# Performance work log

Hardware: AMD Instinct MI355X
Metric: run time of the kernel (lower is better)

## Reference

```python
import jax, jax.numpy as jnp
from jax import lax
import numpy as np

B, C, H, W = 2, 64, 192, 192

def conv2d(x, w, pad):
    return lax.conv_general_dilated(x, w, (1, 1), [(pad, pad), (pad, pad)],
                                    dimension_numbers=('NCHW', 'OIHW', 'NCHW'))

def bilinear_sample(x, py, px):
    # x: [B,C,H,W]; py, px: [B,H,W] absolute fractional coords; zero padding outside.
    Bb, Cc, Hh, Ww = x.shape
    y0 = jnp.floor(py); x0 = jnp.floor(px)
    wy1 = py - y0; wx1 = px - x0
    xf = x.reshape(Bb, Cc, Hh * Ww)
    def gather(yi, xi):
        valid = (yi >= 0) & (yi < Hh) & (xi >= 0) & (xi < Ww)
        yc = jnp.clip(yi, 0, Hh - 1).astype(jnp.int32)
        xc = jnp.clip(xi, 0, Ww - 1).astype(jnp.int32)
        idx = (yc * Ww + xc).reshape(Bb, 1, Hh * Ww)
        v = jnp.take_along_axis(xf, idx, axis=2).reshape(Bb, Cc, Hh, Ww)
        return v * valid[:, None].astype(x.dtype)
    return (gather(y0, x0) * ((1 - wy1) * (1 - wx1))[:, None]
            + gather(y0, x0 + 1) * ((1 - wy1) * wx1)[:, None]
            + gather(y0 + 1, x0) * (wy1 * (1 - wx1))[:, None]
            + gather(y0 + 1, x0 + 1) * (wy1 * wx1)[:, None])

def deform_conv(x, w_off, b_off, w_mod, b_mod, w_reg, k):
    # torchvision deform_conv2d semantics with modulation (mask), stride=1, dilation=1.
    pad = k // 2
    offset = conv2d(x, w_off, pad) + b_off[None, :, None, None]   # [B,2*k*k,H,W] (y,x) interleaved
    mask = 2.0 * jax.nn.sigmoid(conv2d(x, w_mod, pad) + b_mod[None, :, None, None])  # [B,k*k,H,W]
    Bb, Cc, Hh, Ww = x.shape
    gy = jnp.arange(Hh, dtype=x.dtype)[None, :, None]
    gx = jnp.arange(Ww, dtype=x.dtype)[None, None, :]
    out = jnp.zeros((Bb, w_reg.shape[0], Hh, Ww), x.dtype)
    for i in range(k):          # fixed structural loop over kernel taps
        for j in range(k):
            t = i * k + j
            py = gy - pad + i + offset[:, 2 * t]
            px = gx - pad + j + offset[:, 2 * t + 1]
            samp = bilinear_sample(x, py, px) * mask[:, t][:, None]  # [B,C,H,W]
            out = out + jnp.einsum('bchw,oc->bohw', samp, w_reg[:, :, i, j])
    return out

def _branch(x, w_pre, w_off, b_off, w_mod, b_mod, w_reg, k):
    h = jax.nn.relu(conv2d(x, w_pre, 0))  # BasicConv 1x1 + ReLU (no bias)
    return deform_conv(h, w_off, b_off, w_mod, b_mod, w_reg, k)

def _forward(x_max, x_mid, x_small,
             w_pre_max, w_off_max, b_off_max, w_mod_max, b_mod_max, w_reg_max,
             w_pre_mid, w_off_mid, b_off_mid, w_mod_mid, b_mod_mid, w_reg_mid,
             w_pre_small, w_off_small, b_off_small, w_mod_small, b_mod_small, w_reg_small,
             w1, w2):
    y = x_max + x_mid + x_small
    a = _branch(x_max, w_pre_max, w_off_max, b_off_max, w_mod_max, b_mod_max, w_reg_max, 7)
    m = _branch(x_mid, w_pre_mid, w_off_mid, b_off_mid, w_mod_mid, b_mod_mid, w_reg_mid, 5)
    s = _branch(x_small, w_pre_small, w_off_small, b_off_small, w_mod_small, b_mod_small, w_reg_small, 3)
    x = jnp.tanh(m) * a
    x = jax.nn.relu(conv2d(x, w1, 0))
    x = jnp.tanh(s) * x
    x = jax.nn.relu(conv2d(x, w2, 0))
    return x + y

def setup_inputs() -> dict:
    key = jax.random.key(0)
    ks = jax.random.split(key, 32)
    d = {}
    d['x_max'] = jax.random.normal(ks[0], (B, C, H, W), jnp.float32)
    d['x_mid'] = jax.random.normal(ks[1], (B, C, H, W), jnp.float32)
    d['x_small'] = jax.random.normal(ks[2], (B, C, H, W), jnp.float32)
    i = 3
    for name, k in (('max', 7), ('mid', 5), ('small', 3)):
        d[f'w_pre_{name}'] = jax.random.normal(ks[i], (C, C, 1, 1), jnp.float32) * 0.05; i += 1
        d[f'w_off_{name}'] = jax.random.normal(ks[i], (2 * k * k, C, k, k), jnp.float32) * 0.01; i += 1
        d[f'b_off_{name}'] = jax.random.normal(ks[i], (2 * k * k,), jnp.float32) * 0.01; i += 1
        d[f'w_mod_{name}'] = jax.random.normal(ks[i], (k * k, C, k, k), jnp.float32) * 0.01; i += 1
        d[f'b_mod_{name}'] = jax.random.normal(ks[i], (k * k,), jnp.float32) * 0.01; i += 1
        d[f'w_reg_{name}'] = jax.random.normal(ks[i], (C, C, k, k), jnp.float32) * 0.02; i += 1
    d['w1'] = jax.random.normal(ks[i], (C, C, 1, 1), jnp.float32) * 0.05; i += 1
    d['w2'] = jax.random.normal(ks[i], (C, C, 1, 1), jnp.float32) * 0.05
    return d

def reference(x_max, x_mid, x_small,
              w_pre_max, w_off_max, b_off_max, w_mod_max, b_mod_max, w_reg_max,
              w_pre_mid, w_off_mid, b_off_mid, w_mod_mid, b_mod_mid, w_reg_mid,
              w_pre_small, w_off_small, b_off_small, w_mod_small, b_mod_small, w_reg_small,
              w1, w2):
    return _forward(x_max, x_mid, x_small,
                    w_pre_max, w_off_max, b_off_max, w_mod_max, b_mod_max, w_reg_max,
                    w_pre_mid, w_off_mid, b_off_mid, w_mod_mid, b_mod_mid, w_reg_mid,
                    w_pre_small, w_off_small, b_off_small, w_mod_small, b_mod_small, w_reg_small,
                    w1, w2)
```

## Files before the change

kernel.cpp:

```cpp
#include <hip/hip_runtime.h>
#include <hip/hip_bf16.h>
#include <math.h>

#define BB   2
#define CC   64
#define HH   192
#define WW   192
#define HW   (HH*WW)
#define HALO 3
#define HP   (HH + 2*HALO)
#define WP   (WW + 2*HALO)
#define PLANE (HP*WP)

typedef __attribute__((ext_vector_type(8))) _Float16 f16x8;
typedef __attribute__((ext_vector_type(4))) _Float16 f16x4;
typedef __attribute__((ext_vector_type(8))) unsigned short u16x8;
typedef __attribute__((ext_vector_type(4))) float f32x4;

__device__ __forceinline__ float fast_tanh(float x) {
    float e = __expf(2.f * x);
    return 1.f - 2.f * __builtin_amdgcn_rcpf(e + 1.f);
}
__device__ __forceinline__ f16x8 bc16(u16x8 v) { return __builtin_bit_cast(f16x8, v); }

__global__ __launch_bounds__(256) void conv_pre_k(
    const float* __restrict__ X0, const float* __restrict__ X1,
    const float* __restrict__ X2,
    const float* __restrict__ W0, const float* __restrict__ W1,
    const float* __restrict__ W2,
    u16x8* __restrict__ hp8all)
{
    __shared__ float wl[64*32];
    int tid = threadIdx.x;
    int oh  = blockIdx.y;
    int z   = blockIdx.z;
    const float* X = (z == 0) ? X0 : ((z == 1) ? X1 : X2);
    const float* W = (z == 0) ? W0 : ((z == 1) ? W1 : W2);
    u16x8* hp8 = hp8all + (size_t)z * ((size_t)BB*8*PLANE);

    #pragma unroll
    for (int n = 0; n < 8; n++) {
        int idx = tid + n*256;
        int op  = idx >> 6, c = idx & 63;
        wl[c*32 + op] = W[(size_t)(oh*32 + op)*64 + c];
    }
    __syncthreads();

    int p  = blockIdx.x*256 + tid;
    int b  = p / HW;
    int pp = p - b*HW;
    size_t base = (size_t)b*CC*HW + pp;

    float acc[32];
    #pragma unroll
    for (int o = 0; o < 32; o++) acc[o] = 0.f;

    #pragma unroll 4
    for (int c = 0; c < 64; c++) {
        float xv = X[base + (size_t)c*HW];
        const float4* w4 = (const float4*)(wl + c*32);
        #pragma unroll
        for (int q = 0; q < 8; q++) {
            float4 w = w4[q];
            acc[4*q+0] = fmaf(w.x, xv, acc[4*q+0]);
            acc[4*q+1] = fmaf(w.y, xv, acc[4*q+1]);
            acc[4*q+2] = fmaf(w.z, xv, acc[4*q+2]);
            acc[4*q+3] = fmaf(w.w, xv, acc[4*q+3]);
        }
    }

    int y = pp / WW, x = pp - y*WW;
    #pragma unroll
    for (int gq = 0; gq < 4; gq++) {
        u16x8 v;
        #pragma unroll
        for (int c = 0; c < 8; c++)
            v[c] = __builtin_bit_cast(unsigned short,
                     (_Float16)fmaxf(acc[gq*8+c], 0.f));
        hp8[(size_t)(b*8 + oh*4 + gq)*PLANE + (size_t)(y+HALO)*WP + (x+HALO)] = v;
    }
}

template<int MODE>
__global__ __launch_bounds__(256) void conv1x1_k(
    const _Float16* __restrict__ Xv, const _Float16* __restrict__ Mv,
    const float* __restrict__ W,
    const float* __restrict__ Y0, const float* __restrict__ Y1,
    const float* __restrict__ Y2,
    void* __restrict__ outv)
{
    __shared__ float wl[64*32];
    int tid = threadIdx.x;
    int oh  = blockIdx.y;
    #pragma unroll
    for (int n = 0; n < 8; n++) {
        int idx = tid + n*256;
        int op  = idx >> 6, c = idx & 63;
        wl[c*32 + op] = W[(size_t)(oh*32 + op)*64 + c];
    }
    __syncthreads();

    int p  = blockIdx.x*256 + tid;
    int b  = p / HW;
    int pp = p - b*HW;
    size_t base = (size_t)b*CC*HW + pp;

    float acc[32];
    #pragma unroll
    for (int o = 0; o < 32; o++) acc[o] = 0.f;

    #pragma unroll 4
    for (int c = 0; c < 64; c++) {
        float xv = (float)Xv[base + (size_t)c*HW];
        xv *= fast_tanh((float)Mv[base + (size_t)c*HW]);
        const float4* w4 = (const float4*)(wl + c*32);
        #pragma unroll
        for (int q = 0; q < 8; q++) {
            float4 w = w4[q];
            acc[4*q+0] = fmaf(w.x, xv, acc[4*q+0]);
            acc[4*q+1] = fmaf(w.y, xv, acc[4*q+1]);
            acc[4*q+2] = fmaf(w.z, xv, acc[4*q+2]);
            acc[4*q+3] = fmaf(w.w, xv, acc[4*q+3]);
        }
    }

    if (MODE == 1) {
        _Float16* op = (_Float16*)outv + base + (size_t)(oh*32)*HW;
        #pragma unroll
        for (int o = 0; o < 32; o++)
            op[(size_t)o*HW] = (_Float16)fmaxf(acc[o], 0.f);
    } else {
        float* op = (float*)outv + base + (size_t)(oh*32)*HW;
        size_t gi = base + (size_t)(oh*32)*HW;
        #pragma unroll
        for (int o = 0; o < 32; o++) {
            float yv = Y0[gi + (size_t)o*HW] + Y1[gi + (size_t)o*HW] + Y2[gi + (size_t)o*HW];
            op[(size_t)o*HW] = fmaxf(acc[o], 0.f) + yv;
        }
    }
}

template<int K>
__device__ void bake_wtb_dev(const float* __restrict__ Wreg,
                             f16x8* __restrict__ wtb, int t, int tid)
{
    constexpr int KK = K*K;
    for (int e = tid; e < 512; e += 256) {
        int kk = e >> 8, rem = e & 255;
        int ot = rem >> 6, l = rem & 63;
        int lr = l & 15, lg = l >> 4;
        int o  = ot*16 + lr;
        f16x8 v;
        #pragma unroll
        for (int j = 0; j < 8; j++) {
            int c = kk*32 + lg*8 + j;
            v[j] = (_Float16)Wreg[((size_t)o*CC + c)*KK + t];
        }
        wtb[(size_t)t*512 + e] = v;
    }
}
template<int K>
__device__ void bake_wbg_dev(const float* __restrict__ Woff,
                             const float* __restrict__ Wmod,
                             f16x8* __restrict__ wbg, int pos, int tid)
{
    constexpr int KK  = K*K;
    constexpr int NTF = (3*KK + 15)/16;
    for (int idx = tid; idx < 2*NTF*64; idx += 256) {
        int kk  = idx / (NTF*64);
        int rem = idx - kk*(NTF*64);
        int nt  = rem >> 6;
        int l   = rem & 63;
        int lg  = l >> 4, lr = l & 15;
        int n   = nt*16 + lr;
        f16x8 v;
        #pragma unroll
        for (int j = 0; j < 8; j++) {
            int c = kk*32 + lg*8 + j;
            float w = 0.f;
            if (n < 2*KK)      w = Woff[((size_t)n*CC + c)*KK + pos];
            else if (n < 3*KK) w = Wmod[((size_t)(n - 2*KK)*CC + c)*KK + pos];
            v[j] = (_Float16)w;
        }
        wbg[(size_t)pos*(2*NTF*64) + idx] = v;
    }
}
__global__ __launch_bounds__(256) void bake_all_k(
    const float* wreg7, const float* woff7, const float* wmod7,
    const float* wreg5, const float* woff5, const float* wmod5,
    const float* wreg3, const float* woff3, const float* wmod3,
    f16x8* wtb7, f16x8* wbg7, f16x8* wtb5, f16x8* wbg5,
    f16x8* wtb3, f16x8* wbg3)
{
    int blk = blockIdx.x, tid = threadIdx.x;
    if (blk < 49) {
        bake_wtb_dev<7>(wreg7, wtb7, blk, tid);
        bake_wbg_dev<7>(woff7, wmod7, wbg7, blk, tid);
    } else if (blk < 74) {
        int p = blk - 49;
        bake_wtb_dev<5>(wreg5, wtb5, p, tid);
        bake_wbg_dev<5>(woff5, wmod5, wbg5, p, tid);
    } else {
        int p = blk - 74;
        bake_wtb_dev<3>(wreg3, wtb3, p, tid);
        bake_wbg_dev<3>(woff3, wmod3, wbg3, p, tid);
    }
}

template<int K, int MT, int NS, int PPR>
__device__ __forceinline__ void offmod_dev(
    char* smem_raw, int raw,
    const u16x8* __restrict__ hp8,
    const f16x8* __restrict__ wbg,
    const float* __restrict__ Boff, const float* __restrict__ Bmod,
    _Float16* __restrict__ om)
{
    constexpr int PAD  = K/2;
    constexpr int KK   = K*K;
    constexpr int NTF  = (3*KK + 15)/16;
    constexpr int NT   = NTF/NS;
    constexpr int PBB  = HW/(64*MT);
    constexpr int NBLK = BB*PBB*NS;
    constexpr int ROUNDS = (KK + PPR - 1)/PPR;
    constexpr int WELEM  = PPR*2*NT*64;

    f16x8* wl = (f16x8*)smem_raw;

    int swz = (raw & 7)*(NBLK >> 3) + (raw >> 3);
    int ng  = swz % NS;
    int s   = swz / NS;
    int b   = s / PBB;
    int blk = s - b*PBB;

    int tid  = threadIdx.x;
    int wave = tid >> 6;
    int l    = tid & 63;
    int lg   = l >> 4, lr = l & 15;
    int pxw  = blk*(4*MT*16) + wave*(MT*16);
    int y    = pxw / WW, x0 = pxw - y*WW;

    f32x4 acc[MT][NT];
    #pragma unroll
    for (int mt = 0; mt < MT; mt++)
        #pragma unroll
        for (int nt = 0; nt < NT; nt++) acc[mt][nt] = (f32x4)0.f;

    const u16x8* hb = hp8 + (size_t)(b*8)*PLANE;

    for (int r = 0; r < ROUNDS; r++) {
        __syncthreads();
        #pragma unroll
        for (int ii = 0; ii < (WELEM + 255)/256; ii++) {
            int idx = tid + ii*256;
            if (WELEM % 256 == 0 || idx < WELEM) {
                int pp  = idx / (2*NT*64);
                int rem = idx - pp*(2*NT*64);
                int kk  = rem / (NT*64);
                int rem2= rem - kk*(NT*64);
                int nt  = rem2 >> 6;
                int ll  = rem2 & 63;
                int pos = r*PPR + pp;
                if (pos < KK)
                    wl[idx] = wbg[(size_t)pos*(2*NTF*64)
                                  + (size_t)(kk*NTF + ng*NT + nt)*64 + ll];
            }
        }
        __syncthreads();

        #pragma unroll
        for (int pp = 0; pp < PPR; pp++) {
            int pos = r*PPR + pp;
            if (pos >= KK) break;
            int i = pos / K, j = pos - (pos/K)*K;
            int rbase = (y + HALO - PAD + i)*WP + (x0 + HALO - PAD + j);

            #pragma unroll
            for (int kk = 0; kk < 2; kk++) {
                const f16x8* G = (const f16x8*)(hb + (size_t)(kk*4 + lg)*PLANE + rbase);
                f16x8 a[MT];
                #pragma unroll
                for (int mt = 0; mt < MT; mt++) a[mt] = G[mt*16 + lr];
                #pragma unroll
                for (int nt = 0; nt < NT; nt++) {
                    f16x8 bf = wl[((pp*2 + kk)*NT + nt)*64 + l];
                    #pragma unroll
                    for (int mt = 0; mt < MT; mt++)
                        acc[mt][nt] = __builtin_amdgcn_mfma_f32_16x16x32_f16(
                            a[mt], bf, acc[mt][nt], 0, 0, 0);
                }
            }
        }
    }

    #pragma unroll
    for (int nt = 0; nt < NT; nt++) {
        int n = ng*NT*16 + nt*16 + lr;
        if (n < 3*KK) {
            bool is_mask = (n >= 2*KK);
            float bias = is_mask ? Bmod[n - 2*KK] : Boff[n];
            _Float16* dst0 = om + ((size_t)b*3*KK + n)*HW + pxw + lg*4;
            #pragma unroll
            for (int mt = 0; mt < MT; mt++) {
                f32x4 v = acc[mt][nt];
                float v0 = v[0] + bias, v1 = v[1] + bias, v2 = v[2] + bias, v3 = v[3] + bias;
                if (is_mask) {
                    v0 = 2.f * __builtin_amdgcn_rcpf(1.f + __expf(-v0));
                    v1 = 2.f * __builtin_amdgcn_rcpf(1.f + __expf(-v1));
                    v2 = 2.f * __builtin_amdgcn_rcpf(1.f + __expf(-v2));
                    v3 = 2.f * __builtin_amdgcn_rcpf(1.f + __expf(-v3));
                }
                f16x4 o;
                o[0] = (_Float16)v0; o[1] = (_Float16)v1;
                o[2] = (_Float16)v2; o[3] = (_Float16)v3;
                *reinterpret_cast<f16x4*>(dst0 + mt*16) = o;
            }
        }
    }
}

__global__ __launch_bounds__(256) void offmod_all_k(
    const u16x8* __restrict__ hp8,
    const f16x8* __restrict__ wbg7, const f16x8* __restrict__ wbg5,
    const f16x8* __restrict__ wbg3,
    const float* __restrict__ boff7, const float* __restrict__ bmod7,
    const float* __restrict__ boff5, const float* __restrict__ bmod5,
    const float* __restrict__ boff3, const float* __restrict__ bmod3,
    _Float16* __restrict__ om7, _Float16* __restrict__ om5,
    _Float16* __restrict__ om3)
{
    __shared__ __align__(16) char smem[20480];
    constexpr size_t HPB = (size_t)BB*8*PLANE;
    constexpr int G7 = BB*(HW/256)*2;
    constexpr int G5 = BB*(HW/128);
    int blk = blockIdx.x;
    if (blk < G7)
        offmod_dev<7,4,2,2>(smem, blk, hp8, wbg7, boff7, bmod7, om7);
    else if (blk < G7 + G5)
        offmod_dev<5,2,1,2>(smem, blk - G7, hp8 + HPB, wbg5, boff5, bmod5, om5);
    else
        offmod_dev<3,4,1,3>(smem, blk - G7 - G5, hp8 + 2*HPB, wbg3, boff3, bmod3, om3);
}

template<int K> struct DfmLds {
    static constexpr int HWW = K + 2;
    static constexpr int WWW = 16 + K + 2;
    static constexpr int WIN_B = 8*HWW*WWW*16;
    static constexpr int NPT = K*K*16;
    static constexpr int COORD_B = NPT*8 + NPT*4 + ((NPT*2 + 15)/16)*16;
    static constexpr int RED_B = 2*64*16*4;
    static constexpr int UNION_B = (COORD_B > RED_B ? COORD_B : RED_B);
    static constexpr int TOTAL = WIN_B + UNION_B;
};

template<int K>
__device__ __forceinline__ void deform_dev(
    char* smem_raw, int raw,
    const u16x8* __restrict__ hp8,
    const _Float16* __restrict__ om,
    const f16x8* __restrict__ wtb,
    _Float16* __restrict__ out)
{
    constexpr int PAD = K/2;
    constexpr int KK  = K*K;
    constexpr int NSB = HW/16;
    constexpr int HWW = K + 2;
    constexpr int WWW = 16 + K + 2;
    constexpr int WELEMS = 8*HWW*WWW;
    constexpr int NPT = KK*16;

    u16x8* win = (u16x8*)smem_raw;
    char*  ubuf = smem_raw + WELEMS*16;

    f16x4*          hco  = (f16x4*)ubuf;
    unsigned*       gofs = (unsigned*)(ubuf + NPT*8);
    unsigned short* wofs = (unsigned short*)(ubuf + NPT*8 + NPT*4);

    int swz = (raw & 7)*((BB*NSB) >> 3) + (raw >> 3);
    int b = swz / NSB, strip = swz - b*NSB;

    int tid  = threadIdx.x;
    int wave = tid >> 6;
    int l    = tid & 63;
    int lg   = l >> 4;
    int lr   = l & 15;
    int th   = wave & 1;
    int kkh  = wave >> 1;
    int pxbase = strip*16;
    int y    = pxbase / WW;
    int xs   = pxbase - y*WW;

    int wy0 = y  + HALO - PAD - 1;
    int wx0 = xs + HALO - PAD - 1;

    {
        const u16x8* hbb = hp8 + (size_t)(b*8)*PLANE;
        for (int idx = tid; idx < WELEMS; idx += 256) {
            int g  = idx / (HWW*WWW);
            int r2 = idx - g*(HWW*WWW);
            int r  = r2 / WWW;
            int c2 = r2 - r*WWW;
            int gy = min(max(wy0 + r, 0), HP-1);
            int gx = min(max(wx0 + c2, 0), WP-1);
            win[idx] = hbb[(size_t)g*PLANE + gy*WP + gx];
        }
    }
    {
        const _Float16* ob = om + (size_t)b*3*KK*HW + pxbase;
        for (int idx = tid; idx < NPT; idx += 256) {
            int pxl = idx & 15, t = idx >> 4;
            float offy = (float)ob[(size_t)(2*t  )*HW + pxl];
            float offx = (float)ob[(size_t)(2*t+1)*HW + pxl];
            float mk   = (float)ob[(size_t)(2*KK+t)*HW + pxl];
            int i = t / K, j = t - (t/K)*K;
            float py  = (float)(y - PAD + i) + offy;
            float pxf = (float)(xs + pxl - PAD + j) + offx;
            float fy = floorf(py), fx = floorf(pxf);
            float wy1 = py - fy, wx1 = pxf - fx;
            int iy0 = (int)fy, ix0 = (int)fx;
            int Y0 = min(max(iy0, -1), HH) + HALO;
            int X0 = min(max(ix0, -1), WW) + HALO;
            int ry = Y0 - wy0, rx = X0 - wx0;
            bool in = ((unsigned)ry <= (unsigned)(HWW-2)) &
                      ((unsigned)rx <= (unsigned)(WWW-2));
            f16x4 h;
            h[0] = (_Float16)((1.f-wy1)*(1.f-wx1)*mk);
            h[1] = (_Float16)((1.f-wy1)*wx1*mk);
            h[2] = (_Float16)(wy1*(1.f-wx1)*mk);
            h[3] = (_Float16)(wy1*wx1*mk);
            hco[idx]  = h;
            gofs[idx] = (unsigned)(Y0*WP + X0);
            wofs[idx] = (unsigned short)((ry*WWW + rx) | (in ? 0 : 0x8000));
        }
    }
    __syncthreads();

    int t0 = (KK*th)/2, t1 = (KK*(th+1))/2;

    f32x4 acc[4];
    #pragma unroll
    for (int ot = 0; ot < 4; ot++) acc[ot] = (f32x4)0.f;

    const u16x8* hb   = hp8 + (size_t)(b*8 + kkh*4 + lg)*PLANE;
    const u16x8* wing = win + (kkh*4 + lg)*(HWW*WWW);

    #pragma unroll 1
    for (int t = t0; t < t1; t++) {
        int idx = t*16 + lr;
        f16x4 h = hco[idx];
        unsigned short wf = wofs[idx];
        bool in = (wf & 0x8000) == 0;

        f16x8 c0, c1, c2, c3;
        if (__all(in)) {
            const u16x8* Wp = wing + wf;
            c0 = bc16(Wp[0]);   c1 = bc16(Wp[1]);
            c2 = bc16(Wp[WWW]); c3 = bc16(Wp[WWW+1]);
        } else {
            const u16x8* G = hb + gofs[idx];
            c0 = bc16(G[0]);  c1 = bc16(G[1]);
            c2 = bc16(G[WP]); c3 = bc16(G[WP+1]);
        }

        f16x8 s = c0*h[0] + c1*h[1] + c2*h[2] + c3*h[3];

        const f16x8* bp = wtb + (size_t)t*8*64 + l;
        #pragma unroll
        for (int ot = 0; ot < 4; ot++) {
            acc[ot] = __builtin_amdgcn_mfma_f32_16x16x32_f16(
                s, bp[(size_t)(kkh*4 + ot)*64], acc[ot], 0, 0, 0);
        }
    }

    __syncthreads();
    float* redf = (float*)ubuf;
    #define RIDX(tt, o, g)  (((tt)*64 + (o))*16 + (((g) ^ ((o) & 3)) * 4))
    if (kkh == 1) {
        #pragma unroll
        for (int ot = 0; ot < 4; ot++) {
            int o = ot*16 + lr;
            *reinterpret_cast<f32x4*>(&redf[RIDX(th, o, lg)]) = acc[ot];
        }
    }
    __syncthreads();
    if (kkh == 0) {
        #pragma unroll
        for (int ot = 0; ot < 4; ot++) {
            int o = ot*16 + lr;
            acc[ot] += *reinterpret_cast<const f32x4*>(&redf[RIDX(th, o, lg)]);
        }
    }
    __syncthreads();
    if (kkh == 0 && th == 1) {
        #pragma unroll
        for (int ot = 0; ot < 4; ot++) {
            int o = ot*16 + lr;
            *reinterpret_cast<f32x4*>(&redf[RIDX(0, o, lg)]) = acc[ot];
        }
    }
    __syncthreads();
    if (kkh == 0 && th == 0) {
        _Float16* ob = out + (size_t)b*CC*HW + pxbase + lg*4;
        #pragma unroll
        for (int ot = 0; ot < 4; ot++) {
            int o = ot*16 + lr;
            f32x4 rr = *reinterpret_cast<const f32x4*>(&redf[RIDX(0, o, lg)]);
            rr += acc[ot];
            f16x4 v;
            v[0] = (_Float16)rr[0]; v[1] = (_Float16)rr[1];
            v[2] = (_Float16)rr[2]; v[3] = (_Float16)rr[3];
            *reinterpret_cast<f16x4*>(ob + (size_t)o*HW) = v;
        }
    }
    #undef RIDX
}

__global__ __launch_bounds__(256, 4) void deform_all_k(
    const u16x8* __restrict__ hp8,
    const _Float16* __restrict__ om7, const _Float16* __restrict__ om5,
    const _Float16* __restrict__ om3,
    const f16x8* __restrict__ wtb7, const f16x8* __restrict__ wtb5,
    const f16x8* __restrict__ wtb3,
    _Float16* __restrict__ aa, _Float16* __restrict__ mm,
    _Float16* __restrict__ sm)
{
    constexpr int DFM_SMEM =
        (DfmLds<7>::TOTAL > DfmLds<5>::TOTAL ?
            (DfmLds<7>::TOTAL > DfmLds<3>::TOTAL ? DfmLds<7>::TOTAL : DfmLds<3>::TOTAL)
          : (DfmLds<5>::TOTAL > DfmLds<3>::TOTAL ? DfmLds<5>::TOTAL : DfmLds<3>::TOTAL));
    __shared__ __align__(16) char smem[DFM_SMEM];
    constexpr size_t HPB = (size_t)BB*8*PLANE;
    constexpr int GD = BB*(HW/16);
    int blk = blockIdx.x;
    if (blk < GD)
        deform_dev<7>(smem, blk, hp8, om7, wtb7, aa);
    else if (blk < 2*GD)
        deform_dev<5>(smem, blk - GD, hp8 + HPB, om5, wtb5, mm);
    else
        deform_dev<3>(smem, blk - 2*GD, hp8 + 2*HPB, om3, wtb3, sm);
}

extern "C" void kernel_launch(void* const* d_in, const int* in_sizes, int n_in,
                              void* d_out, int out_size, void* d_ws, size_t ws_size,
                              hipStream_t stream)
{
    const float* x_max      = (const float*)d_in[0];
    const float* x_mid      = (const float*)d_in[1];
    const float* x_small    = (const float*)d_in[2];
    const float* w_pre_max  = (const float*)d_in[3];
    const float* w_off_max  = (const float*)d_in[4];
    const float* b_off_max  = (const float*)d_in[5];
    const float* w_mod_max  = (const float*)d_in[6];
    const float* b_mod_max  = (const float*)d_in[7];
    const float* w_reg_max  = (const float*)d_in[8];
    const float* w_pre_mid  = (const float*)d_in[9];
    const float* w_off_mid  = (const float*)d_in[10];
    const float* b_off_mid  = (const float*)d_in[11];
    const float* w_mod_mid  = (const float*)d_in[12];
    const float* b_mod_mid  = (const float*)d_in[13];
    const float* w_reg_mid  = (const float*)d_in[14];
    const float* w_pre_small= (const float*)d_in[15];
    const float* w_off_small= (const float*)d_in[16];
    const float* b_off_small= (const float*)d_in[17];
    const float* w_mod_small= (const float*)d_in[18];
    const float* b_mod_small= (const float*)d_in[19];
    const float* w_reg_small= (const float*)d_in[20];
    const float* w1         = (const float*)d_in[21];
    const float* w2         = (const float*)d_in[22];

    float* out = (float*)d_out;
    char*  ws  = (char*)d_ws;

    const size_t HPB = (size_t)BB*8*PLANE;

    u16x8*    hp8 = (u16x8*)ws;                 ws += 3*HPB*16;
    _Float16* om7 = (_Float16*)ws;              ws += (size_t)BB*3*49*HW*2;
    _Float16* om5 = (_Float16*)ws;              ws += (size_t)BB*3*25*HW*2;
    _Float16* om3 = (_Float16*)ws;              ws += (size_t)BB*3*9*HW*2;
    _Float16* aa  = (_Float16*)ws;              ws += (size_t)BB*CC*HW*2;
    _Float16* mm  = (_Float16*)ws;              ws += (size_t)BB*CC*HW*2;
    _Float16* sm  = (_Float16*)ws;              ws += (size_t)BB*CC*HW*2;
    f16x8*    wtb7= (f16x8*)ws;                 ws += (size_t)49*512*16;
    f16x8*    wbg7= (f16x8*)ws;                 ws += (size_t)49*2*10*64*16;
    f16x8*    wtb5= (f16x8*)ws;                 ws += (size_t)25*512*16;
    f16x8*    wbg5= (f16x8*)ws;                 ws += (size_t)25*2*5*64*16;
    f16x8*    wtb3= (f16x8*)ws;                 ws += (size_t)9*512*16;
    f16x8*    wbg3= (f16x8*)ws;
    _Float16* u   = om7;

    hipMemsetAsync(hp8, 0, 3*HPB*16, stream);

    const int npix_blocks = (BB*HW)/256;
    const int off_blocks  = BB*(HW/256)*2 + BB*(HW/128) + BB*(HW/256);
    const int dfm_blocks  = 3*BB*(HW/16);

    bake_all_k<<<83, 256, 0, stream>>>(
        w_reg_max, w_off_max, w_mod_max,
        w_reg_mid, w_off_mid, w_mod_mid,
        w_reg_small, w_off_small, w_mod_small,
        wtb7, wbg7, wtb5, wbg5, wtb3, wbg3);
    conv_pre_k<<<dim3(npix_blocks, 2, 3), 256, 0, stream>>>(
        x_max, x_mid, x_small, w_pre_max, w_pre_mid, w_pre_small, hp8);

    offmod_all_k<<<off_blocks, 256, 0, stream>>>(
        hp8, wbg7, wbg5, wbg3,
        b_off_max, b_mod_max, b_off_mid, b_mod_mid, b_off_small, b_mod_small,
        om7, om5, om3);

    deform_all_k<<<dfm_blocks, 256, 0, stream>>>(
        hp8, om7, om5, om3, wtb7, wtb5, wtb3, aa, mm, sm);

    conv1x1_k<1><<<dim3(npix_blocks,2), 256, 0, stream>>>(aa, mm, w1,
                                                  nullptr, nullptr, nullptr, u);
    conv1x1_k<2><<<dim3(npix_blocks,2), 256, 0, stream>>>(u, sm, w2,
                                                  x_max, x_mid, x_small, out);
}
```

Before: 383.4 us.

## Fuse the two trailing 1x1 convolutions into one kernel via shared memory

The two back-to-back 1x1 conv kernels are merged into a single 512-thread kernel. Each block computes the intermediate u tile for 256 pixels across all 64 channels, keeps it in LDS instead of writing it to global memory, then applies the second gated 1x1 conv and the residual sum. This removes a global round trip of the intermediate tensor and one kernel launch. Weights are stored in LDS as fp16, which adds a small precision loss. Separately, the deform kernel's tap loop is unrolled by 2.

```diff
diff --git a/kernel.cpp b/kernel.cpp
--- a/kernel.cpp
+++ b/kernel.cpp
@@ -81,26 +81,29 @@
     }
 }
 
-template<int MODE>
-__global__ __launch_bounds__(256) void conv1x1_k(
-    const _Float16* __restrict__ Xv, const _Float16* __restrict__ Mv,
-    const float* __restrict__ W,
-    const float* __restrict__ Y0, const float* __restrict__ Y1,
-    const float* __restrict__ Y2,
-    void* __restrict__ outv)
-{
-    __shared__ float wl[64*32];
+__global__ __launch_bounds__(512) void combine_k(
+    const _Float16* __restrict__ aa, const _Float16* __restrict__ mm,
+    const _Float16* __restrict__ sm,
+    const float* __restrict__ X0, const float* __restrict__ X1,
+    const float* __restrict__ X2,
+    const float* __restrict__ W1, const float* __restrict__ W2,
+    float* __restrict__ out)
+{
+    __shared__ _Float16 ul[64][256];
+    __shared__ _Float16 w1l[64][64];
+    __shared__ _Float16 w2l[64][64];
+
     int tid = threadIdx.x;
-    int oh  = blockIdx.y;
-    #pragma unroll
-    for (int n = 0; n < 8; n++) {
-        int idx = tid + n*256;
-        int op  = idx >> 6, c = idx & 63;
-        wl[c*32 + op] = W[(size_t)(oh*32 + op)*64 + c];
-    }
-    __syncthreads();
-
-    int p  = blockIdx.x*256 + tid;
+    for (int i = tid; i < 4096; i += 512) {
+        int o = i >> 6, c = i & 63;
+        w1l[c][o] = (_Float16)W1[i];
+        w2l[c][o] = (_Float16)W2[i];
+    }
+    __syncthreads();
+
+    int oh = tid >> 8;
+    int t  = tid & 255;
+    int p  = blockIdx.x*256 + t;
     int b  = p / HW;
     int pp = p - b*HW;
     size_t base = (size_t)b*CC*HW + pp;
@@ -111,32 +114,37 @@
 
     #pragma unroll 4
     for (int c = 0; c < 64; c++) {
-        float xv = (float)Xv[base + (size_t)c*HW];
-        xv *= fast_tanh((float)Mv[base + (size_t)c*HW]);
-        const float4* w4 = (const float4*)(wl + c*32);
-        #pragma unroll
-        for (int q = 0; q < 8; q++) {
-            float4 w = w4[q];
-            acc[4*q+0] = fmaf(w.x, xv, acc[4*q+0]);
-            acc[4*q+1] = fmaf(w.y, xv, acc[4*q+1]);
-            acc[4*q+2] = fmaf(w.z, xv, acc[4*q+2]);
-            acc[4*q+3] = fmaf(w.w, xv, acc[4*q+3]);
-        }
-    }
-
-    if (MODE == 1) {
-        _Float16* op = (_Float16*)outv + base + (size_t)(oh*32)*HW;
+        float xv = (float)aa[base + (size_t)c*HW]
+                 * fast_tanh((float)mm[base + (size_t)c*HW]);
+        const _Float16* w = &w1l[c][oh*32];
         #pragma unroll
         for (int o = 0; o < 32; o++)
-            op[(size_t)o*HW] = (_Float16)fmaxf(acc[o], 0.f);
-    } else {
-        float* op = (float*)outv + base + (size_t)(oh*32)*HW;
-        size_t gi = base + (size_t)(oh*32)*HW;
-        #pragma unroll
-        for (int o = 0; o < 32; o++) {
-            float yv = Y0[gi + (size_t)o*HW] + Y1[gi + (size_t)o*HW] + Y2[gi + (size_t)o*HW];
-            op[(size_t)o*HW] = fmaxf(acc[o], 0.f) + yv;
-        }
+            acc[o] = fmaf((float)w[o], xv, acc[o]);
+    }
+    #pragma unroll
+    for (int o = 0; o < 32; o++)
+        ul[oh*32 + o][t] = (_Float16)fmaxf(acc[o], 0.f);
+    __syncthreads();
+
+    #pragma unroll
+    for (int o = 0; o < 32; o++) acc[o] = 0.f;
+
+    #pragma unroll 4
+    for (int c = 0; c < 64; c++) {
+        float uv = (float)ul[c][t]
+                 * fast_tanh((float)sm[base + (size_t)c*HW]);
+        const _Float16* w = &w2l[c][oh*32];
+        #pragma unroll
+        for (int o = 0; o < 32; o++)
+            acc[o] = fmaf((float)w[o], uv, acc[o]);
+    }
+
+    size_t gi = base + (size_t)(oh*32)*HW;
+    #pragma unroll
+    for (int o = 0; o < 32; o++) {
+        float yv = X0[gi + (size_t)o*HW] + X1[gi + (size_t)o*HW]
+                 + X2[gi + (size_t)o*HW];
+        out[gi + (size_t)o*HW] = fmaxf(acc[o], 0.f) + yv;
     }
 }
 
@@ -443,7 +451,7 @@
     const u16x8* hb   = hp8 + (size_t)(b*8 + kkh*4 + lg)*PLANE;
     const u16x8* wing = win + (kkh*4 + lg)*(HWW*WWW);
 
-    #pragma unroll 1
+    #pragma unroll 2
     for (int t = t0; t < t1; t++) {
         int idx = t*16 + lr;
         f16x4 h = hco[idx];
@@ -585,7 +593,6 @@
     f16x8*    wbg5= (f16x8*)ws;                 ws += (size_t)25*2*5*64*16;
     f16x8*    wtb3= (f16x8*)ws;                 ws += (size_t)9*512*16;
     f16x8*    wbg3= (f16x8*)ws;
-    _Float16* u   = om7;
 
     hipMemsetAsync(hp8, 0, 3*HPB*16, stream);
 
@@ -609,8 +616,6 @@
     deform_all_k<<<dfm_blocks, 256, 0, stream>>>(
         hp8, om7, om5, om3, wtb7, wtb5, wtb3, aa, mm, sm);
 
-    conv1x1_k<1><<<dim3(npix_blocks,2), 256, 0, stream>>>(aa, mm, w1,
-                                                  nullptr, nullptr, nullptr, u);
-    conv1x1_k<2><<<dim3(npix_blocks,2), 256, 0, stream>>>(u, sm, w2,
-                                                  x_max, x_mid, x_small, out);
-}
+    combine_k<<<npix_blocks, 512, 0, stream>>>(
+        aa, mm, sm, x_max, x_mid, x_small, w1, w2, out);
+}
```

After: 431.6 us. +12.6%, slower.
